# Optimization experiments

Hardware: AMD Instinct MI355X
Metric: run time of the kernel (lower is better)

The kernel has to match this reference:

```python
import jax, jax.numpy as jnp
import numpy as np

B, N, D = 1, 2048, 512        # batch, query seq len, model dim
H, DH = 8, 64                 # heads, head dim
MEM = 512                     # cached XL memory tokens (one window segment)
KV = N + MEM                  # kv sequence length
WINDOW = 512                  # block / sliding-window size
LOOKBACK = 1                  # lookback_blocks
N_EP = 4                      # number of episodes
SCALE = DH ** -0.5


def _rope(t, pos):
    # t: [b,h,l,dh], pos: [l]  (GPT-NeoX half rotation)
    dh = t.shape[-1]
    inv_freq = 1.0 / (10000.0 ** (jnp.arange(0, dh, 2, dtype=jnp.float32) / dh))
    freqs = pos.astype(jnp.float32)[:, None] * inv_freq[None, :]   # [l, dh/2]
    freqs = jnp.concatenate([freqs, freqs], axis=-1)               # [l, dh]
    cos, sin = jnp.cos(freqs), jnp.sin(freqs)
    x1, x2 = jnp.split(t, 2, axis=-1)
    rotated = jnp.concatenate([-x2, x1], axis=-1)
    return t * cos + rotated * sin


def setup_inputs() -> dict:
    key = jax.random.key(0)
    ks = jax.random.split(key, 8)
    x = jax.random.normal(ks[0], (B, N, D), jnp.float32)
    cache_k = jax.random.normal(ks[1], (B, H, MEM, DH), jnp.float32)
    cache_v = jax.random.normal(ks[2], (B, H, MEM, DH), jnp.float32)
    episode_ids = jnp.sort(jax.random.randint(ks[3], (B, KV), 0, N_EP, dtype=jnp.int32), axis=-1)
    Wq = jax.random.normal(ks[4], (D, H * DH), jnp.float32) * 0.02
    Wkv = jax.random.normal(ks[5], (D, 2 * H * DH), jnp.float32) * 0.02
    Wg = jax.random.normal(ks[6], (D, H), jnp.float32) * 0.02
    Wo = jax.random.normal(ks[7], (H * DH, D), jnp.float32) * 0.02
    return dict(x=x, cache_k=cache_k, cache_v=cache_v, episode_ids=episode_ids,
                Wq=Wq, Wkv=Wkv, Wg=Wg, Wo=Wo)


def _xl_mask(episode_ids):
    # mirrors create_xl_mask: causal + block window with lookback + intra-episode
    offset = KV - N
    q_pos = offset + jnp.arange(N)          # [N]
    k_pos = jnp.arange(KV)                  # [KV]
    causal = q_pos[:, None] >= k_pos[None, :]
    bq = q_pos // WINDOW
    bk = k_pos // WINDOW
    block = (bq[:, None] >= bk[None, :]) & (bq[:, None] <= bk[None, :] + LOOKBACK)
    intra_ep = episode_ids[:, q_pos][:, :, None] == episode_ids[:, None, :]  # [B,N,KV]
    return (causal & block)[None] & intra_ep                                 # [B,N,KV]


def reference(x, cache_k, cache_v, episode_ids, Wq, Wkv, Wg, Wo):
    b, n, _ = x.shape
    offset = KV - N

    q = (x @ Wq).reshape(b, n, H, DH).transpose(0, 2, 1, 3)          # [b,h,n,dh]
    kv = (x @ Wkv).reshape(b, n, 2, H, DH)
    k_new = kv[:, :, 0].transpose(0, 2, 1, 3)                        # [b,h,n,dh]
    v_new = kv[:, :, 1].transpose(0, 2, 1, 3)

    k = jnp.concatenate([cache_k, k_new], axis=2)                    # [b,h,kv,dh]
    v = jnp.concatenate([cache_v, v_new], axis=2)

    q = _rope(q, offset + jnp.arange(n))
    k = _rope(k, jnp.arange(KV))

    scores = jnp.einsum('bhnd,bhmd->bhnm', q, k) * SCALE             # [b,h,n,kv]
    mask = _xl_mask(episode_ids)[:, None]                            # [b,1,n,kv]
    scores = jnp.where(mask, scores, jnp.finfo(scores.dtype).min)
    attn = jax.nn.softmax(scores, axis=-1)

    out = jnp.einsum('bhnm,bhmd->bhnd', attn, v)                     # [b,h,n,dh]

    gates = jax.nn.sigmoid(x @ Wg).transpose(0, 2, 1)[..., None]     # [b,h,n,1]
    out = out * gates

    out = out.transpose(0, 2, 1, 3).reshape(b, n, H * DH)            # merge heads
    return out @ Wo                                                  # [b,n,d]
```

## Files before the change

kernel.cpp:

```cpp
#include <hip/hip_runtime.h>
#include <math.h>

#define NQ     2048
#define DMODEL 512
#define NH     8
#define DHD    64
#define MEMT   512
#define KVT    2560
#define QSCALE 0.125f
#define NEGF   (-1e30f)

typedef unsigned short u16;
typedef __bf16 bf16x8 __attribute__((ext_vector_type(8)));
typedef float  f32x4  __attribute__((ext_vector_type(4)));
typedef u16    u16x8  __attribute__((ext_vector_type(8)));
typedef u16    u16x4  __attribute__((ext_vector_type(4)));

__device__ __forceinline__ u16 f2bf(float f) {
    union { float f; unsigned u; } v; v.f = f;
    unsigned r = (v.u + 0x7FFFu + ((v.u >> 16) & 1u)) >> 16;
    return (u16)r;
}

__global__ __launch_bounds__(256) void prep(const float* __restrict__ x,
                                            const float* __restrict__ Wq,
                                            const float* __restrict__ Wkv,
                                            const float* __restrict__ Wo,
                                            const float* __restrict__ Wg,
                                            u16* __restrict__ xb,
                                            u16* __restrict__ Wt,
                                            u16* __restrict__ Wot,
                                            float* __restrict__ gates,
                                            float2* __restrict__ cs) {
    __shared__ float tile[64][65];
    int bx = blockIdx.x, tid = threadIdx.x;

    if (bx >= 384) {
        int t = (bx - 384) * 256 + tid;
        int pos = t >> 5, j = t & 31;
        float invf = exp2f(-(float)j * (13.287712379549449f / 32.f));
        float ss, sc;
        sincosf((float)pos * invf, &ss, &sc);
        cs[t] = make_float2(sc, ss);
        return;
    }
    if (bx >= 320) {
        int t = (bx - 320) * 256 + tid;
        int n = t >> 3, hh = t & 7;
        float acc = 0.f;
        for (int k = 0; k < DMODEL; k += 4) {
            float4 xv = *(const float4*)&x[n * DMODEL + k];
            acc += xv.x * Wg[(k + 0) * NH + hh] + xv.y * Wg[(k + 1) * NH + hh]
                 + xv.z * Wg[(k + 2) * NH + hh] + xv.w * Wg[(k + 3) * NH + hh];
        }
        gates[hh * NQ + n] = 1.f / (1.f + __expf(-acc));
        return;
    }
    if (bx < 64) {
        int base4 = bx * 4096;
#pragma unroll
        for (int u = 0; u < 16; ++u) {
            int i4 = base4 + u * 256 + tid;
            float4 v = ((const float4*)x)[i4];
            u16x4 o = { f2bf(v.x), f2bf(v.y), f2bf(v.z), f2bf(v.w) };
            *(u16x4*)&xb[i4 * 4] = o;
        }
        return;
    }
    int tt = bx - 64;
    bool isQKV = (tt < 192);
    int tc, tr;
    if (isQKV) { tc = tt % 24; tr = tt / 24; }
    else       { tt -= 192; tc = tt & 7; tr = tt >> 3; }

    int rr = tid >> 4, c4 = (tid & 15) * 4;
#pragma unroll
    for (int u = 0; u < 4; ++u) {
        int row = u * 16 + rr;
        int k = tr * 64 + row;
        int c = tc * 64 + c4;
        float4 v;
        if (isQKV) v = (c < 512) ? *(const float4*)&Wq[k * 512 + c]
                                 : *(const float4*)&Wkv[k * 1024 + (c - 512)];
        else       v = *(const float4*)&Wo[k * 512 + c];
        tile[row][c4 + 0] = v.x; tile[row][c4 + 1] = v.y;
        tile[row][c4 + 2] = v.z; tile[row][c4 + 3] = v.w;
    }
    __syncthreads();
#pragma unroll
    for (int u = 0; u < 4; ++u) {
        int trow = u * 16 + rr;
        u16x4 o;
#pragma unroll
        for (int i = 0; i < 4; ++i) o[i] = f2bf(tile[c4 + i][trow]);
        int t_glob = tc * 64 + trow;
        int k_glob = tr * 64 + c4;
        if (isQKV) *(u16x4*)&Wt[t_glob * 512 + k_glob] = o;
        else       *(u16x4*)&Wot[t_glob * 512 + k_glob] = o;
    }
}

__global__ __launch_bounds__(256) void kv_prep(const float* __restrict__ cache_k,
                                               const float* __restrict__ cache_v,
                                               const u16* __restrict__ vn,
                                               const float2* __restrict__ cs,
                                               u16* __restrict__ kb,
                                               u16* __restrict__ vt) {
    __shared__ u16 tile[64][66];
    int h = blockIdx.y, bx = blockIdx.x;
    int tid = threadIdx.x;

    if (bx < 8) {
        int r0 = bx * 64;
#pragma unroll
        for (int u = 0; u < 8; ++u) {
            int idx = u * 256 + tid;
            int row = idx >> 5, j = idx & 31;
            int r = r0 + row;
            float a = cache_k[(h * MEMT + r) * DHD + j];
            float b = cache_k[(h * MEMT + r) * DHD + 32 + j];
            float2 csv = cs[r * 32 + j];
            kb[(h * KVT + r) * DHD + j]      = f2bf(a * csv.x - b * csv.y);
            kb[(h * KVT + r) * DHD + 32 + j] = f2bf(b * csv.x + a * csv.y);
        }
        return;
    }

    int tb = bx - 8;
    int rr = tid >> 4, c4 = (tid & 15) * 4;
    if (tb < 8) {
        int r0 = tb * 64;
#pragma unroll
        for (int u = 0; u < 4; ++u) {
            int row = u * 16 + rr;
            float4 v = *(const float4*)&cache_v[(h * MEMT + r0 + row) * DHD + c4];
            tile[row][c4 + 0] = f2bf(v.x); tile[row][c4 + 1] = f2bf(v.y);
            tile[row][c4 + 2] = f2bf(v.z); tile[row][c4 + 3] = f2bf(v.w);
        }
    } else {
        int n0 = (tb - 8) * 64;
#pragma unroll
        for (int u = 0; u < 4; ++u) {
            int row = u * 16 + rr;
            u16x4 v = *(const u16x4*)&vn[(h * NQ + n0 + row) * DHD + c4];
            tile[row][c4 + 0] = v[0]; tile[row][c4 + 1] = v[1];
            tile[row][c4 + 2] = v[2]; tile[row][c4 + 3] = v[3];
        }
    }
    __syncthreads();
    int kvbase = tb * 64;
#pragma unroll
    for (int u = 0; u < 4; ++u) {
        int d = u * 16 + rr;
        u16x4 o = { tile[c4 + 0][d], tile[c4 + 1][d], tile[c4 + 2][d], tile[c4 + 3][d] };
        *(u16x4*)&vt[(h * DHD + d) * KVT + kvbase + c4] = o;
    }
}

template<int MODE>
__global__ __launch_bounds__(256) void gemm_mfma(const u16* __restrict__ A,
                                                 const u16* __restrict__ Bt,
                                                 const float2* __restrict__ cs,
                                                 u16* __restrict__ o_q,
                                                 u16* __restrict__ o_k,
                                                 u16* __restrict__ o_v,
                                                 float* __restrict__ o_f) {
    int bx = blockIdx.x, by = blockIdx.y;
    int tid = threadIdx.x;
    int w = tid >> 6, lane = tid & 63;
    int lr = lane & 15, lg = lane >> 4;
    int rowbase = by * 64 + (w >> 1) * 32;
    int colbase = bx * 64 + (w & 1) * 16;

    f32x4 acc[2][2];
#pragma unroll
    for (int i = 0; i < 2; ++i)
#pragma unroll
        for (int j = 0; j < 2; ++j) { f32x4 z = {0.f, 0.f, 0.f, 0.f}; acc[i][j] = z; }

    const u16* a0 = A + (rowbase + lr) * 512 + lg * 8;
    const u16* a1 = a0 + 16 * 512;
    const u16* b0 = Bt + (colbase + lr) * 512 + lg * 8;
    const u16* b1 = b0 + 32 * 512;

#pragma unroll 4
    for (int k0 = 0; k0 < 512; k0 += 32) {
        bf16x8 fa0 = __builtin_bit_cast(bf16x8, *(const u16x8*)(a0 + k0));
        bf16x8 fa1 = __builtin_bit_cast(bf16x8, *(const u16x8*)(a1 + k0));
        bf16x8 fb0 = __builtin_bit_cast(bf16x8, *(const u16x8*)(b0 + k0));
        bf16x8 fb1 = __builtin_bit_cast(bf16x8, *(const u16x8*)(b1 + k0));
        acc[0][0] = __builtin_amdgcn_mfma_f32_16x16x32_bf16(fa0, fb0, acc[0][0], 0, 0, 0);
        acc[0][1] = __builtin_amdgcn_mfma_f32_16x16x32_bf16(fa0, fb1, acc[0][1], 0, 0, 0);
        acc[1][0] = __builtin_amdgcn_mfma_f32_16x16x32_bf16(fa1, fb0, acc[1][0], 0, 0, 0);
        acc[1][1] = __builtin_amdgcn_mfma_f32_16x16x32_bf16(fa1, fb1, acc[1][1], 0, 0, 0);
    }

    if (MODE == 1) {
#pragma unroll
        for (int rt = 0; rt < 2; ++rt)
#pragma unroll
            for (int r = 0; r < 4; ++r) {
                int n = rowbase + rt * 16 + lg * 4 + r;
                o_f[n * DMODEL + colbase + lr]      = acc[rt][0][r];
                o_f[n * DMODEL + colbase + 32 + lr] = acc[rt][1][r];
            }
        return;
    }

    int j = (colbase & 63) + lr;
    int region = bx >> 3;
    int h = bx & 7;
#pragma unroll
    for (int rt = 0; rt < 2; ++rt)
#pragma unroll
        for (int r = 0; r < 4; ++r) {
            int n = rowbase + rt * 16 + lg * 4 + r;
            float a = acc[rt][0][r], b = acc[rt][1][r];
            if (region == 2) {
                o_v[(h * NQ + n) * DHD + j]      = f2bf(a);
                o_v[(h * NQ + n) * DHD + 32 + j] = f2bf(b);
            } else {
                float2 csv = cs[(512 + n) * 32 + j];
                u16 e0 = f2bf(a * csv.x - b * csv.y);
                u16 e1 = f2bf(b * csv.x + a * csv.y);
                if (region == 0) {
                    o_q[(h * NQ + n) * DHD + j]      = e0;
                    o_q[(h * NQ + n) * DHD + 32 + j] = e1;
                } else {
                    o_k[(h * KVT + 512 + n) * DHD + j]      = e0;
                    o_k[(h * KVT + 512 + n) * DHD + 32 + j] = e1;
                }
            }
        }
}

#define LOADK(BK, BEP, C0)                                                     \
  _Pragma("unroll")                                                            \
  for (int t = 0; t < 4; ++t) {                                                \
    const u16* kr = kb + ((h * KVT + (C0) + t * 16 + lr) * DHD + lg * 8);      \
    BK[t][0] = __builtin_bit_cast(bf16x8, *(const u16x8*)kr);                  \
    BK[t][1] = __builtin_bit_cast(bf16x8, *(const u16x8*)(kr + 32));           \
    BEP[t] = ep[(C0) + t * 16 + lr];                                           \
  }

#define DO_CHUNK(C0, BK, BEP, PREF, NBK, NBEP)                                 \
  {                                                                            \
    bf16x8 bV[4][2];                                                           \
    _Pragma("unroll")                                                          \
    for (int t = 0; t < 4; ++t) {                                              \
      const u16* vr = vtb + ((h * DHD + t * 16 + lr) * KVT + (C0) + lg * 8);   \
      bV[t][0] = __builtin_bit_cast(bf16x8, *(const u16x8*)vr);                \
      bV[t][1] = __builtin_bit_cast(bf16x8, *(const u16x8*)(vr + 32));         \
    }                                                                          \
    f32x4 s[4];                                                                \
    _Pragma("unroll")                                                          \
    for (int t = 0; t < 4; ++t) {                                              \
      f32x4 z = {0.f, 0.f, 0.f, 0.f};                                          \
      s[t] = __builtin_amdgcn_mfma_f32_16x16x32_bf16(aQ[0], BK[t][0], z, 0, 0, 0); \
      s[t] = __builtin_amdgcn_mfma_f32_16x16x32_bf16(aQ[1], BK[t][1], s[t], 0, 0, 0); \
    }                                                                          \
    if (PREF) { LOADK(NBK, NBEP, (C0) + 64) }                                  \
    float rmax[4] = {NEGF, NEGF, NEGF, NEGF};                                  \
    _Pragma("unroll")                                                          \
    for (int t = 0; t < 4; ++t) {                                              \
      int key = (C0) + t * 16 + lr;                                            \
      int ek = BEP[t];                                                         \
      _Pragma("unroll")                                                        \
      for (int r = 0; r < 4; ++r) {                                            \
        bool vld = (key <= qpos[r]) && (ek == epq[r]);                         \
        float sv = vld ? s[t][r] * QSCALE : NEGF;                              \
        s[t][r] = sv;                                                          \
        rmax[r] = fmaxf(rmax[r], sv);                                          \
      }                                                                        \
    }                                                                          \
    _Pragma("unroll")                                                          \
    for (int mm = 1; mm < 16; mm <<= 1) {                                      \
      _Pragma("unroll")                                                        \
      for (int r = 0; r < 4; ++r)                                              \
        rmax[r] = fmaxf(rmax[r], __shfl_xor(rmax[r], mm, 64));                 \
    }                                                                          \
    float alpha[4];                                                            \
    _Pragma("unroll")                                                          \
    for (int r = 0; r < 4; ++r) {                                              \
      float mn = fmaxf(mrun[r], rmax[r]);                                      \
      alpha[r] = __expf(mrun[r] - mn);                                         \
      mrun[r] = mn;                                                            \
      lsum[r] *= alpha[r];                                                     \
    }                                                                          \
    _Pragma("unroll")                                                          \
    for (int t = 0; t < 4; ++t)                                                \
      _Pragma("unroll")                                                        \
      for (int r = 0; r < 4; ++r) o[t][r] *= alpha[r];                         \
    float psum[4] = {0.f, 0.f, 0.f, 0.f};                                      \
    _Pragma("unroll")                                                          \
    for (int t = 0; t < 4; ++t) {                                              \
      _Pragma("unroll")                                                        \
      for (int r = 0; r < 4; ++r) {                                            \
        float sv = s[t][r];                                                    \
        float p = (sv <= -1e29f) ? 0.f : __expf(sv - mrun[r]);                 \
        psum[r] += p;                                                          \
        int qq = lg * 4 + r;                                                   \
        int kk2 = t * 16 + lr;                                                 \
        pl[qq * 64 + (kk2 ^ ((qq & 7) << 3))] = f2bf(p);                       \
      }                                                                        \
    }                                                                          \
    _Pragma("unroll")                                                          \
    for (int mm = 1; mm < 16; mm <<= 1) {                                      \
      _Pragma("unroll")                                                        \
      for (int r = 0; r < 4; ++r) psum[r] += __shfl_xor(psum[r], mm, 64);      \
    }                                                                          \
    _Pragma("unroll")                                                          \
    for (int r = 0; r < 4; ++r) lsum[r] += psum[r];                            \
    bf16x8 aP[2];                                                              \
    {                                                                          \
      int sw = (lr & 7) << 3;                                                  \
      aP[0] = __builtin_bit_cast(bf16x8, *(const u16x8*)&pl[lr * 64 + ((lg * 8) ^ sw)]);        \
      aP[1] = __builtin_bit_cast(bf16x8, *(const u16x8*)&pl[lr * 64 + ((32 + lg * 8) ^ sw)]);   \
    }                                                                          \
    _Pragma("unroll")                                                          \
    for (int t = 0; t < 4; ++t) {                                              \
      o[t] = __builtin_amdgcn_mfma_f32_16x16x32_bf16(aP[0], bV[t][0], o[t], 0, 0, 0); \
      o[t] = __builtin_amdgcn_mfma_f32_16x16x32_bf16(aP[1], bV[t][1], o[t], 0, 0, 0); \
    }                                                                          \
  }

__global__ __launch_bounds__(256, 2) void attn_mfma(const u16* __restrict__ qb,
                                                    const u16* __restrict__ kb,
                                                    const u16* __restrict__ vtb,
                                                    const float* __restrict__ gates,
                                                    const int* __restrict__ ep,
                                                    u16* __restrict__ outp) {
    __shared__ u16 plds[4][16 * 64];
    __shared__ float o_l[2][16][68];
    __shared__ float ml_l[2][2][16];

    int h = blockIdx.y;
    int q0 = blockIdx.x * 32;
    int tid = threadIdx.x;
    int w = tid >> 6, lane = tid & 63;
    int lr = lane & 15, lg = lane >> 4;
    int qsub = w & 1, kvh = w >> 1;
    int qbase = q0 + qsub * 16;
    u16* pl = plds[w];

    bf16x8 aQ[2];
    {
        const u16* qrow = qb + ((h * NQ + qbase + lr) * DHD + lg * 8);
        aQ[0] = __builtin_bit_cast(bf16x8, *(const u16x8*)qrow);
        aQ[1] = __builtin_bit_cast(bf16x8, *(const u16x8*)(qrow + 32));
    }

    int qpos[4], epq[4];
    float gq[4];
#pragma unroll
    for (int r = 0; r < 4; ++r) {
        int q = qbase + lg * 4 + r;
        qpos[r] = 512 + q;
        epq[r] = ep[512 + q];
        gq[r] = gates[h * NQ + q];
    }

    f32x4 o[4];
    float mrun[4], lsum[4];
#pragma unroll
    for (int t = 0; t < 4; ++t) { f32x4 z = {0.f,0.f,0.f,0.f}; o[t] = z; }
#pragma unroll
    for (int r = 0; r < 4; ++r) { mrun[r] = NEGF; lsum[r] = 0.f; }

    int c_lo = q0 & ~511;
    int nch = (544 + (q0 & 511) + 63) >> 6;
    int n0 = nch >> 1;
    int my_n = kvh ? (nch - n0) : n0;
    int c0 = c_lo + (kvh ? (n0 << 6) : 0);

    bf16x8 bKA[4][2], bKB[4][2];
    int epA[4], epB[4];

    LOADK(bKA, epA, c0)
    int ci = 0;
    while (true) {
        bool more = (ci + 1 < my_n);
        DO_CHUNK(c0, bKA, epA, more, bKB, epB)
        ++ci; c0 += 64;
        if (!more) break;
        bool more2 = (ci + 1 < my_n);
        DO_CHUNK(c0, bKB, epB, more2, bKA, epA)
        ++ci; c0 += 64;
        if (!more2) break;
    }

    if (kvh == 1) {
#pragma unroll
        for (int r = 0; r < 4; ++r) {
            ml_l[qsub][0][lg * 4 + r] = mrun[r];
            ml_l[qsub][1][lg * 4 + r] = lsum[r];
        }
#pragma unroll
        for (int t = 0; t < 4; ++t)
#pragma unroll
            for (int r = 0; r < 4; ++r)
                o_l[qsub][lg * 4 + r][t * 16 + lr] = o[t][r];
    }
    __syncthreads();
    if (kvh == 0) {
#pragma unroll
        for (int r = 0; r < 4; ++r) {
            int row = lg * 4 + r;
            float m1 = ml_l[qsub][0][row], l1 = ml_l[qsub][1][row];
            float m0 = mrun[r], l0 = lsum[r];
            float mm2 = fmaxf(m0, m1);
            float f0 = (m0 <= -1e29f) ? 0.f : __expf(m0 - mm2);
            float f1 = (m1 <= -1e29f) ? 0.f : __expf(m1 - mm2);
            float lt = l0 * f0 + l1 * f1;
            float inv = gq[r] / lt;
            int q = qbase + row;
#pragma unroll
            for (int t = 0; t < 4; ++t) {
                float o1 = o_l[qsub][row][t * 16 + lr];
                outp[q * DMODEL + h * DHD + t * 16 + lr] =
                    f2bf((o[t][r] * f0 + o1 * f1) * inv);
            }
        }
    }
}

extern "C" void kernel_launch(void* const* d_in, const int* in_sizes, int n_in,
                              void* d_out, int out_size, void* d_ws, size_t ws_size,
                              hipStream_t stream) {
    const float* x       = (const float*)d_in[0];
    const float* cache_k = (const float*)d_in[1];
    const float* cache_v = (const float*)d_in[2];
    const int*   ep      = (const int*)  d_in[3];
    const float* Wq      = (const float*)d_in[4];
    const float* Wkv     = (const float*)d_in[5];
    const float* Wg      = (const float*)d_in[6];
    const float* Wo      = (const float*)d_in[7];
    float* out = (float*)d_out;

    u16* u = (u16*)d_ws;
    u16* x_bf    = u;
    u16* Wt      = x_bf + 1048576;
    u16* Wot     = Wt + 786432;
    u16* q_bf    = Wot + 262144;
    u16* k_bf    = q_bf + 1048576;
    u16* vn_bf   = k_bf + 1310720;
    u16* vT      = vn_bf + 1048576;
    u16* attn_bf = vT + 1310720;
    float*  gatesw = (float*)(attn_bf + 1048576);
    float2* cs     = (float2*)(gatesw + 16384);

    prep<<<704, 256, 0, stream>>>(x, Wq, Wkv, Wo, Wg, x_bf, Wt, Wot, gatesw, cs);
    gemm_mfma<0><<<dim3(24, 32), 256, 0, stream>>>(x_bf, Wt, cs, q_bf, k_bf, vn_bf, nullptr);
    kv_prep<<<dim3(48, 8), 256, 0, stream>>>(cache_k, cache_v, vn_bf, cs, k_bf, vT);
    attn_mfma<<<dim3(64, 8), 256, 0, stream>>>(q_bf, k_bf, vT, gatesw, ep, attn_bf);
    gemm_mfma<1><<<dim3(8, 32), 256, 0, stream>>>(attn_bf, Wot, nullptr, nullptr, nullptr, nullptr, out);
}
```

Baseline: 154.8 us.

## Fuse all stages into one persistent kernel with software grid barriers

Replaces the five separate kernel launches (prep, QKV GEMM, kv_prep, attention, output GEMM) with a single persistent kernel of 512 blocks. Phases are separated by a flag-based grid barrier in global memory. The QKV GEMM epilogue now writes V directly in transposed layout, which removes the intermediate vn buffer and its separate transpose pass. The goal is to cut launch overhead and inter-kernel gaps. In exchange it relies on all 512 blocks being co-resident, adds barrier spin cost, and reuses flags tags across calls.

```diff
diff --git a/kernel.cpp b/kernel.cpp
--- a/kernel.cpp
+++ b/kernel.cpp
@@ -9,6 +9,7 @@
 #define KVT    2560
 #define QSCALE 0.125f
 #define NEGF   (-1e30f)
+#define NBLK   512
 
 typedef unsigned short u16;
 typedef __bf16 bf16x8 __attribute__((ext_vector_type(8)));
@@ -22,216 +23,33 @@
     return (u16)r;
 }
 
-__global__ __launch_bounds__(256) void prep(const float* __restrict__ x,
-                                            const float* __restrict__ Wq,
-                                            const float* __restrict__ Wkv,
-                                            const float* __restrict__ Wo,
-                                            const float* __restrict__ Wg,
-                                            u16* __restrict__ xb,
-                                            u16* __restrict__ Wt,
-                                            u16* __restrict__ Wot,
-                                            float* __restrict__ gates,
-                                            float2* __restrict__ cs) {
-    __shared__ float tile[64][65];
-    int bx = blockIdx.x, tid = threadIdx.x;
-
-    if (bx >= 384) {
-        int t = (bx - 384) * 256 + tid;
-        int pos = t >> 5, j = t & 31;
-        float invf = exp2f(-(float)j * (13.287712379549449f / 32.f));
-        float ss, sc;
-        sincosf((float)pos * invf, &ss, &sc);
-        cs[t] = make_float2(sc, ss);
-        return;
-    }
-    if (bx >= 320) {
-        int t = (bx - 320) * 256 + tid;
-        int n = t >> 3, hh = t & 7;
-        float acc = 0.f;
-        for (int k = 0; k < DMODEL; k += 4) {
-            float4 xv = *(const float4*)&x[n * DMODEL + k];
-            acc += xv.x * Wg[(k + 0) * NH + hh] + xv.y * Wg[(k + 1) * NH + hh]
-                 + xv.z * Wg[(k + 2) * NH + hh] + xv.w * Wg[(k + 3) * NH + hh];
-        }
-        gates[hh * NQ + n] = 1.f / (1.f + __expf(-acc));
-        return;
-    }
-    if (bx < 64) {
-        int base4 = bx * 4096;
-#pragma unroll
-        for (int u = 0; u < 16; ++u) {
-            int i4 = base4 + u * 256 + tid;
-            float4 v = ((const float4*)x)[i4];
-            u16x4 o = { f2bf(v.x), f2bf(v.y), f2bf(v.z), f2bf(v.w) };
-            *(u16x4*)&xb[i4 * 4] = o;
-        }
-        return;
-    }
-    int tt = bx - 64;
-    bool isQKV = (tt < 192);
-    int tc, tr;
-    if (isQKV) { tc = tt % 24; tr = tt / 24; }
-    else       { tt -= 192; tc = tt & 7; tr = tt >> 3; }
-
-    int rr = tid >> 4, c4 = (tid & 15) * 4;
-#pragma unroll
-    for (int u = 0; u < 4; ++u) {
-        int row = u * 16 + rr;
-        int k = tr * 64 + row;
-        int c = tc * 64 + c4;
-        float4 v;
-        if (isQKV) v = (c < 512) ? *(const float4*)&Wq[k * 512 + c]
-                                 : *(const float4*)&Wkv[k * 1024 + (c - 512)];
-        else       v = *(const float4*)&Wo[k * 512 + c];
-        tile[row][c4 + 0] = v.x; tile[row][c4 + 1] = v.y;
-        tile[row][c4 + 2] = v.z; tile[row][c4 + 3] = v.w;
+__device__ __forceinline__ void gridbar(int* flags, int tag) {
+    __syncthreads();
+    int bid = blockIdx.x, tid = threadIdx.x;
+    if (tid == 0)
+        __hip_atomic_store(&flags[bid], tag, __ATOMIC_RELEASE, __HIP_MEMORY_SCOPE_AGENT);
+    if (bid == 0) {
+        __shared__ int nd;
+        for (;;) {
+            if (tid == 0) nd = 0;
+            __syncthreads();
+            int bad = 0;
+            for (int j = tid; j < NBLK; j += 256)
+                if (__hip_atomic_load(&flags[j], __ATOMIC_ACQUIRE, __HIP_MEMORY_SCOPE_AGENT) != tag) { bad = 1; break; }
+            if (bad) nd = 1;
+            __syncthreads();
+            if (nd == 0) break;
+            __builtin_amdgcn_s_sleep(2);
+        }
+        if (tid == 0)
+            __hip_atomic_store(&flags[NBLK], tag, __ATOMIC_RELEASE, __HIP_MEMORY_SCOPE_AGENT);
+    } else {
+        if (tid == 0) {
+            while (__hip_atomic_load(&flags[NBLK], __ATOMIC_ACQUIRE, __HIP_MEMORY_SCOPE_AGENT) != tag)
+                __builtin_amdgcn_s_sleep(2);
+        }
     }
     __syncthreads();
-#pragma unroll
-    for (int u = 0; u < 4; ++u) {
-        int trow = u * 16 + rr;
-        u16x4 o;
-#pragma unroll
-        for (int i = 0; i < 4; ++i) o[i] = f2bf(tile[c4 + i][trow]);
-        int t_glob = tc * 64 + trow;
-        int k_glob = tr * 64 + c4;
-        if (isQKV) *(u16x4*)&Wt[t_glob * 512 + k_glob] = o;
-        else       *(u16x4*)&Wot[t_glob * 512 + k_glob] = o;
-    }
-}
-
-__global__ __launch_bounds__(256) void kv_prep(const float* __restrict__ cache_k,
-                                               const float* __restrict__ cache_v,
-                                               const u16* __restrict__ vn,
-                                               const float2* __restrict__ cs,
-                                               u16* __restrict__ kb,
-                                               u16* __restrict__ vt) {
-    __shared__ u16 tile[64][66];
-    int h = blockIdx.y, bx = blockIdx.x;
-    int tid = threadIdx.x;
-
-    if (bx < 8) {
-        int r0 = bx * 64;
-#pragma unroll
-        for (int u = 0; u < 8; ++u) {
-            int idx = u * 256 + tid;
-            int row = idx >> 5, j = idx & 31;
-            int r = r0 + row;
-            float a = cache_k[(h * MEMT + r) * DHD + j];
-            float b = cache_k[(h * MEMT + r) * DHD + 32 + j];
-            float2 csv = cs[r * 32 + j];
-            kb[(h * KVT + r) * DHD + j]      = f2bf(a * csv.x - b * csv.y);
-            kb[(h * KVT + r) * DHD + 32 + j] = f2bf(b * csv.x + a * csv.y);
-        }
-        return;
-    }
-
-    int tb = bx - 8;
-    int rr = tid >> 4, c4 = (tid & 15) * 4;
-    if (tb < 8) {
-        int r0 = tb * 64;
-#pragma unroll
-        for (int u = 0; u < 4; ++u) {
-            int row = u * 16 + rr;
-            float4 v = *(const float4*)&cache_v[(h * MEMT + r0 + row) * DHD + c4];
-            tile[row][c4 + 0] = f2bf(v.x); tile[row][c4 + 1] = f2bf(v.y);
-            tile[row][c4 + 2] = f2bf(v.z); tile[row][c4 + 3] = f2bf(v.w);
-        }
-    } else {
-        int n0 = (tb - 8) * 64;
-#pragma unroll
-        for (int u = 0; u < 4; ++u) {
-            int row = u * 16 + rr;
-            u16x4 v = *(const u16x4*)&vn[(h * NQ + n0 + row) * DHD + c4];
-            tile[row][c4 + 0] = v[0]; tile[row][c4 + 1] = v[1];
-            tile[row][c4 + 2] = v[2]; tile[row][c4 + 3] = v[3];
-        }
-    }
-    __syncthreads();
-    int kvbase = tb * 64;
-#pragma unroll
-    for (int u = 0; u < 4; ++u) {
-        int d = u * 16 + rr;
-        u16x4 o = { tile[c4 + 0][d], tile[c4 + 1][d], tile[c4 + 2][d], tile[c4 + 3][d] };
-        *(u16x4*)&vt[(h * DHD + d) * KVT + kvbase + c4] = o;
-    }
-}
-
-template<int MODE>
-__global__ __launch_bounds__(256) void gemm_mfma(const u16* __restrict__ A,
-                                                 const u16* __restrict__ Bt,
-                                                 const float2* __restrict__ cs,
-                                                 u16* __restrict__ o_q,
-                                                 u16* __restrict__ o_k,
-                                                 u16* __restrict__ o_v,
-                                                 float* __restrict__ o_f) {
-    int bx = blockIdx.x, by = blockIdx.y;
-    int tid = threadIdx.x;
-    int w = tid >> 6, lane = tid & 63;
-    int lr = lane & 15, lg = lane >> 4;
-    int rowbase = by * 64 + (w >> 1) * 32;
-    int colbase = bx * 64 + (w & 1) * 16;
-
-    f32x4 acc[2][2];
-#pragma unroll
-    for (int i = 0; i < 2; ++i)
-#pragma unroll
-        for (int j = 0; j < 2; ++j) { f32x4 z = {0.f, 0.f, 0.f, 0.f}; acc[i][j] = z; }
-
-    const u16* a0 = A + (rowbase + lr) * 512 + lg * 8;
-    const u16* a1 = a0 + 16 * 512;
-    const u16* b0 = Bt + (colbase + lr) * 512 + lg * 8;
-    const u16* b1 = b0 + 32 * 512;
-
-#pragma unroll 4
-    for (int k0 = 0; k0 < 512; k0 += 32) {
-        bf16x8 fa0 = __builtin_bit_cast(bf16x8, *(const u16x8*)(a0 + k0));
-        bf16x8 fa1 = __builtin_bit_cast(bf16x8, *(const u16x8*)(a1 + k0));
-        bf16x8 fb0 = __builtin_bit_cast(bf16x8, *(const u16x8*)(b0 + k0));
-        bf16x8 fb1 = __builtin_bit_cast(bf16x8, *(const u16x8*)(b1 + k0));
-        acc[0][0] = __builtin_amdgcn_mfma_f32_16x16x32_bf16(fa0, fb0, acc[0][0], 0, 0, 0);
-        acc[0][1] = __builtin_amdgcn_mfma_f32_16x16x32_bf16(fa0, fb1, acc[0][1], 0, 0, 0);
-        acc[1][0] = __builtin_amdgcn_mfma_f32_16x16x32_bf16(fa1, fb0, acc[1][0], 0, 0, 0);
-        acc[1][1] = __builtin_amdgcn_mfma_f32_16x16x32_bf16(fa1, fb1, acc[1][1], 0, 0, 0);
-    }
-
-    if (MODE == 1) {
-#pragma unroll
-        for (int rt = 0; rt < 2; ++rt)
-#pragma unroll
-            for (int r = 0; r < 4; ++r) {
-                int n = rowbase + rt * 16 + lg * 4 + r;
-                o_f[n * DMODEL + colbase + lr]      = acc[rt][0][r];
-                o_f[n * DMODEL + colbase + 32 + lr] = acc[rt][1][r];
-            }
-        return;
-    }
-
-    int j = (colbase & 63) + lr;
-    int region = bx >> 3;
-    int h = bx & 7;
-#pragma unroll
-    for (int rt = 0; rt < 2; ++rt)
-#pragma unroll
-        for (int r = 0; r < 4; ++r) {
-            int n = rowbase + rt * 16 + lg * 4 + r;
-            float a = acc[rt][0][r], b = acc[rt][1][r];
-            if (region == 2) {
-                o_v[(h * NQ + n) * DHD + j]      = f2bf(a);
-                o_v[(h * NQ + n) * DHD + 32 + j] = f2bf(b);
-            } else {
-                float2 csv = cs[(512 + n) * 32 + j];
-                u16 e0 = f2bf(a * csv.x - b * csv.y);
-                u16 e1 = f2bf(b * csv.x + a * csv.y);
-                if (region == 0) {
-                    o_q[(h * NQ + n) * DHD + j]      = e0;
-                    o_q[(h * NQ + n) * DHD + 32 + j] = e1;
-                } else {
-                    o_k[(h * KVT + 512 + n) * DHD + j]      = e0;
-                    o_k[(h * KVT + 512 + n) * DHD + 32 + j] = e1;
-                }
-            }
-        }
 }
 
 #define LOADK(BK, BEP, C0)                                                     \
@@ -324,102 +142,307 @@
     }                                                                          \
   }
 
-__global__ __launch_bounds__(256, 2) void attn_mfma(const u16* __restrict__ qb,
-                                                    const u16* __restrict__ kb,
-                                                    const u16* __restrict__ vtb,
-                                                    const float* __restrict__ gates,
-                                                    const int* __restrict__ ep,
-                                                    u16* __restrict__ outp) {
-    __shared__ u16 plds[4][16 * 64];
-    __shared__ float o_l[2][16][68];
-    __shared__ float ml_l[2][2][16];
-
-    int h = blockIdx.y;
-    int q0 = blockIdx.x * 32;
-    int tid = threadIdx.x;
-    int w = tid >> 6, lane = tid & 63;
-    int lr = lane & 15, lg = lane >> 4;
-    int qsub = w & 1, kvh = w >> 1;
-    int qbase = q0 + qsub * 16;
-    u16* pl = plds[w];
-
-    bf16x8 aQ[2];
+__global__ __launch_bounds__(256, 2) void mega(
+    const float* __restrict__ x, const float* __restrict__ cache_k,
+    const float* __restrict__ cache_v, const int* __restrict__ ep,
+    const float* __restrict__ Wq, const float* __restrict__ Wkv,
+    const float* __restrict__ Wg, const float* __restrict__ Wo,
+    u16* __restrict__ xb, u16* __restrict__ Wt, u16* __restrict__ Wot,
+    u16* __restrict__ qb, u16* __restrict__ kb, u16* __restrict__ vtb,
+    u16* __restrict__ attnb, float* __restrict__ gates,
+    float2* __restrict__ cs, int* __restrict__ flags,
+    float* __restrict__ outf)
+{
+    __shared__ char smem[17408];
+    const int bid = blockIdx.x, tid = threadIdx.x;
+    const int w = tid >> 6, lane = tid & 63;
+    const int lr = lane & 15, lg = lane >> 4;
+
+    for (int unit = bid; unit < 576; unit += NBLK) {
+        if (unit < 64) {
+            int base4 = unit * 4096;
+#pragma unroll
+            for (int u = 0; u < 16; ++u) {
+                int i4 = base4 + u * 256 + tid;
+                float4 v = ((const float4*)x)[i4];
+                u16x4 o4 = { f2bf(v.x), f2bf(v.y), f2bf(v.z), f2bf(v.w) };
+                *(u16x4*)&xb[i4 * 4] = o4;
+            }
+        } else if (unit < 320) {
+            __syncthreads();
+            float (*tile)[65] = (float(*)[65])smem;
+            int tt = unit - 64;
+            bool isQKV = (tt < 192);
+            int tc, tr;
+            if (isQKV) { tc = tt % 24; tr = tt / 24; }
+            else       { tt -= 192; tc = tt & 7; tr = tt >> 3; }
+            int rr = tid >> 4, c4 = (tid & 15) * 4;
+#pragma unroll
+            for (int u = 0; u < 4; ++u) {
+                int row = u * 16 + rr;
+                int k = tr * 64 + row, c = tc * 64 + c4;
+                float4 v;
+                if (isQKV) v = (c < 512) ? *(const float4*)&Wq[k * 512 + c]
+                                         : *(const float4*)&Wkv[k * 1024 + (c - 512)];
+                else       v = *(const float4*)&Wo[k * 512 + c];
+                tile[row][c4 + 0] = v.x; tile[row][c4 + 1] = v.y;
+                tile[row][c4 + 2] = v.z; tile[row][c4 + 3] = v.w;
+            }
+            __syncthreads();
+#pragma unroll
+            for (int u = 0; u < 4; ++u) {
+                int trow = u * 16 + rr;
+                u16x4 o4;
+#pragma unroll
+                for (int i = 0; i < 4; ++i) o4[i] = f2bf(tile[c4 + i][trow]);
+                int tg = tc * 64 + trow, kg = tr * 64 + c4;
+                if (isQKV) *(u16x4*)&Wt[tg * 512 + kg] = o4;
+                else       *(u16x4*)&Wot[tg * 512 + kg] = o4;
+            }
+        } else if (unit < 384) {
+            int t = (unit - 320) * 256 + tid;
+            int n = t >> 3, hh = t & 7;
+            float acc = 0.f;
+            for (int k = 0; k < DMODEL; k += 4) {
+                float4 xv = *(const float4*)&x[n * DMODEL + k];
+                acc += xv.x * Wg[(k + 0) * NH + hh] + xv.y * Wg[(k + 1) * NH + hh]
+                     + xv.z * Wg[(k + 2) * NH + hh] + xv.w * Wg[(k + 3) * NH + hh];
+            }
+            gates[hh * NQ + n] = 1.f / (1.f + __expf(-acc));
+        } else if (unit < 512) {
+            int tu = unit - 384;
+#pragma unroll
+            for (int kk = 0; kk < 3; ++kk) {
+                int e = kk * 256 + tid;
+                if (e < 640) {
+                    int idx = tu * 640 + e;
+                    int pos = idx >> 5, j = idx & 31;
+                    float invf = exp2f(-(float)j * (13.287712379549449f / 32.f));
+                    float ss, sc;
+                    sincosf((float)pos * invf, &ss, &sc);
+                    cs[idx] = make_float2(sc, ss);
+                }
+            }
+        } else {
+            __syncthreads();
+            u16 (*tile)[66] = (u16(*)[66])smem;
+            int uu = unit - 512;
+            int tb = uu & 7, h = uu >> 3;
+            int rr = tid >> 4, c4 = (tid & 15) * 4;
+            int r0 = tb * 64;
+#pragma unroll
+            for (int u = 0; u < 4; ++u) {
+                int row = u * 16 + rr;
+                float4 v = *(const float4*)&cache_v[(h * MEMT + r0 + row) * DHD + c4];
+                tile[row][c4 + 0] = f2bf(v.x); tile[row][c4 + 1] = f2bf(v.y);
+                tile[row][c4 + 2] = f2bf(v.z); tile[row][c4 + 3] = f2bf(v.w);
+            }
+            __syncthreads();
+#pragma unroll
+            for (int u = 0; u < 4; ++u) {
+                int d = u * 16 + rr;
+                u16x4 o4 = { tile[c4 + 0][d], tile[c4 + 1][d], tile[c4 + 2][d], tile[c4 + 3][d] };
+                *(u16x4*)&vtb[(h * DHD + d) * KVT + r0 + c4] = o4;
+            }
+        }
+    }
+    gridbar(flags, 0x7A5A0001);
+
+    for (int u2 = bid; u2 < 832; u2 += NBLK) {
+        if (u2 < 768) {
+            int bx = u2 % 24, by = u2 / 24;
+            int rowbase = by * 64 + (w >> 1) * 32;
+            int colbase = bx * 64 + (w & 1) * 16;
+            f32x4 acc[2][2];
+#pragma unroll
+            for (int i = 0; i < 2; ++i)
+#pragma unroll
+                for (int j = 0; j < 2; ++j) { f32x4 z = {0.f,0.f,0.f,0.f}; acc[i][j] = z; }
+            const u16* a0 = xb + (rowbase + lr) * 512 + lg * 8;
+            const u16* a1 = a0 + 16 * 512;
+            const u16* b0 = Wt + (colbase + lr) * 512 + lg * 8;
+            const u16* b1 = b0 + 32 * 512;
+#pragma unroll 4
+            for (int k0 = 0; k0 < 512; k0 += 32) {
+                bf16x8 fa0 = __builtin_bit_cast(bf16x8, *(const u16x8*)(a0 + k0));
+                bf16x8 fa1 = __builtin_bit_cast(bf16x8, *(const u16x8*)(a1 + k0));
+                bf16x8 fb0 = __builtin_bit_cast(bf16x8, *(const u16x8*)(b0 + k0));
+                bf16x8 fb1 = __builtin_bit_cast(bf16x8, *(const u16x8*)(b1 + k0));
+                acc[0][0] = __builtin_amdgcn_mfma_f32_16x16x32_bf16(fa0, fb0, acc[0][0], 0, 0, 0);
+                acc[0][1] = __builtin_amdgcn_mfma_f32_16x16x32_bf16(fa0, fb1, acc[0][1], 0, 0, 0);
+                acc[1][0] = __builtin_amdgcn_mfma_f32_16x16x32_bf16(fa1, fb0, acc[1][0], 0, 0, 0);
+                acc[1][1] = __builtin_amdgcn_mfma_f32_16x16x32_bf16(fa1, fb1, acc[1][1], 0, 0, 0);
+            }
+            int j = (colbase & 63) + lr;
+            int region = bx >> 3;
+            int h = bx & 7;
+            if (region == 2) {
+                __syncthreads();
+                u16 (*vtile)[72] = (u16(*)[72])smem;
+#pragma unroll
+                for (int rt = 0; rt < 2; ++rt)
+#pragma unroll
+                    for (int r = 0; r < 4; ++r) {
+                        int rl = (w >> 1) * 32 + rt * 16 + lg * 4 + r;
+                        vtile[rl][j]      = f2bf(acc[rt][0][r]);
+                        vtile[rl][j + 32] = f2bf(acc[rt][1][r]);
+                    }
+                __syncthreads();
+                int rr = tid >> 4, c4 = (tid & 15) * 4;
+#pragma unroll
+                for (int u = 0; u < 4; ++u) {
+                    int d = u * 16 + rr;
+                    u16x4 o4 = { vtile[c4 + 0][d], vtile[c4 + 1][d], vtile[c4 + 2][d], vtile[c4 + 3][d] };
+                    *(u16x4*)&vtb[(h * DHD + d) * KVT + 512 + by * 64 + c4] = o4;
+                }
+            } else {
+#pragma unroll
+                for (int rt = 0; rt < 2; ++rt)
+#pragma unroll
+                    for (int r = 0; r < 4; ++r) {
+                        int n = rowbase + rt * 16 + lg * 4 + r;
+                        float a = acc[rt][0][r], b = acc[rt][1][r];
+                        float2 csv = cs[(512 + n) * 32 + j];
+                        u16 e0 = f2bf(a * csv.x - b * csv.y);
+                        u16 e1 = f2bf(b * csv.x + a * csv.y);
+                        if (region == 0) {
+                            qb[(h * NQ + n) * DHD + j]      = e0;
+                            qb[(h * NQ + n) * DHD + 32 + j] = e1;
+                        } else {
+                            kb[(h * KVT + 512 + n) * DHD + j]      = e0;
+                            kb[(h * KVT + 512 + n) * DHD + 32 + j] = e1;
+                        }
+                    }
+            }
+        } else {
+            int uu = u2 - 768;
+            int r0 = (uu & 7) * 64, h = uu >> 3;
+#pragma unroll
+            for (int u = 0; u < 8; ++u) {
+                int idx = u * 256 + tid;
+                int row = idx >> 5, j = idx & 31;
+                int r = r0 + row;
+                float a = cache_k[(h * MEMT + r) * DHD + j];
+                float b = cache_k[(h * MEMT + r) * DHD + 32 + j];
+                float2 csv = cs[r * 32 + j];
+                kb[(h * KVT + r) * DHD + j]      = f2bf(a * csv.x - b * csv.y);
+                kb[(h * KVT + r) * DHD + 32 + j] = f2bf(b * csv.x + a * csv.y);
+            }
+        }
+    }
+    gridbar(flags, 0x7A5A0002);
+
     {
-        const u16* qrow = qb + ((h * NQ + qbase + lr) * DHD + lg * 8);
-        aQ[0] = __builtin_bit_cast(bf16x8, *(const u16x8*)qrow);
-        aQ[1] = __builtin_bit_cast(bf16x8, *(const u16x8*)(qrow + 32));
+        u16* plds = (u16*)smem;
+        float* o_lf = (float*)(smem + 8192);
+        float* ml_lf = (float*)(smem + 16896);
+        int h = bid >> 6;
+        int q0 = (bid & 63) * 32;
+        int qsub = w & 1, kvh = w >> 1;
+        int qbase = q0 + qsub * 16;
+        u16* pl = plds + w * 1024;
+
+        bf16x8 aQ[2];
+        {
+            const u16* qrow = qb + ((h * NQ + qbase + lr) * DHD + lg * 8);
+            aQ[0] = __builtin_bit_cast(bf16x8, *(const u16x8*)qrow);
+            aQ[1] = __builtin_bit_cast(bf16x8, *(const u16x8*)(qrow + 32));
+        }
+        int qpos[4], epq[4];
+        float gq[4];
+#pragma unroll
+        for (int r = 0; r < 4; ++r) {
+            int q = qbase + lg * 4 + r;
+            qpos[r] = 512 + q;
+            epq[r] = ep[512 + q];
+            gq[r] = gates[h * NQ + q];
+        }
+        f32x4 o[4];
+        float mrun[4], lsum[4];
+#pragma unroll
+        for (int t = 0; t < 4; ++t) { f32x4 z = {0.f,0.f,0.f,0.f}; o[t] = z; }
+#pragma unroll
+        for (int r = 0; r < 4; ++r) { mrun[r] = NEGF; lsum[r] = 0.f; }
+
+        int c_lo = q0 & ~511;
+        int nch = (544 + (q0 & 511) + 63) >> 6;
+        int n0 = nch >> 1;
+        int my_n = kvh ? (nch - n0) : n0;
+        int c0 = c_lo + (kvh ? (n0 << 6) : 0);
+
+        bf16x8 bKA[4][2], bKB[4][2];
+        int epA[4], epB[4];
+        LOADK(bKA, epA, c0)
+        int ci = 0;
+        while (true) {
+            bool more = (ci + 1 < my_n);
+            DO_CHUNK(c0, bKA, epA, more, bKB, epB)
+            ++ci; c0 += 64;
+            if (!more) break;
+            bool more2 = (ci + 1 < my_n);
+            DO_CHUNK(c0, bKB, epB, more2, bKA, epA)
+            ++ci; c0 += 64;
+            if (!more2) break;
+        }
+
+        if (kvh == 1) {
+#pragma unroll
+            for (int r = 0; r < 4; ++r) {
+                ml_lf[(qsub * 2 + 0) * 16 + lg * 4 + r] = mrun[r];
+                ml_lf[(qsub * 2 + 1) * 16 + lg * 4 + r] = lsum[r];
+            }
+#pragma unroll
+            for (int t = 0; t < 4; ++t)
+#pragma unroll
+                for (int r = 0; r < 4; ++r)
+                    o_lf[(qsub * 16 + lg * 4 + r) * 68 + t * 16 + lr] = o[t][r];
+        }
+        __syncthreads();
+        if (kvh == 0) {
+#pragma unroll
+            for (int r = 0; r < 4; ++r) {
+                int row = lg * 4 + r;
+                float m1 = ml_lf[(qsub * 2 + 0) * 16 + row];
+                float l1 = ml_lf[(qsub * 2 + 1) * 16 + row];
+                float m0 = mrun[r], l0 = lsum[r];
+                float mm2 = fmaxf(m0, m1);
+                float f0 = (m0 <= -1e29f) ? 0.f : __expf(m0 - mm2);
+                float f1 = (m1 <= -1e29f) ? 0.f : __expf(m1 - mm2);
+                float lt = l0 * f0 + l1 * f1;
+                float inv = gq[r] / lt;
+                int q = qbase + row;
+#pragma unroll
+                for (int t = 0; t < 4; ++t) {
+                    float o1 = o_lf[(qsub * 16 + row) * 68 + t * 16 + lr];
+                    attnb[q * DMODEL + h * DHD + t * 16 + lr] =
+                        f2bf((o[t][r] * f0 + o1 * f1) * inv);
+                }
+            }
+        }
     }
-
-    int qpos[4], epq[4];
-    float gq[4];
-#pragma unroll
-    for (int r = 0; r < 4; ++r) {
-        int q = qbase + lg * 4 + r;
-        qpos[r] = 512 + q;
-        epq[r] = ep[512 + q];
-        gq[r] = gates[h * NQ + q];
-    }
-
-    f32x4 o[4];
-    float mrun[4], lsum[4];
-#pragma unroll
-    for (int t = 0; t < 4; ++t) { f32x4 z = {0.f,0.f,0.f,0.f}; o[t] = z; }
-#pragma unroll
-    for (int r = 0; r < 4; ++r) { mrun[r] = NEGF; lsum[r] = 0.f; }
-
-    int c_lo = q0 & ~511;
-    int nch = (544 + (q0 & 511) + 63) >> 6;
-    int n0 = nch >> 1;
-    int my_n = kvh ? (nch - n0) : n0;
-    int c0 = c_lo + (kvh ? (n0 << 6) : 0);
-
-    bf16x8 bKA[4][2], bKB[4][2];
-    int epA[4], epB[4];
-
-    LOADK(bKA, epA, c0)
-    int ci = 0;
-    while (true) {
-        bool more = (ci + 1 < my_n);
-        DO_CHUNK(c0, bKA, epA, more, bKB, epB)
-        ++ci; c0 += 64;
-        if (!more) break;
-        bool more2 = (ci + 1 < my_n);
-        DO_CHUNK(c0, bKB, epB, more2, bKA, epA)
-        ++ci; c0 += 64;
-        if (!more2) break;
-    }
-
-    if (kvh == 1) {
+    gridbar(flags, 0x7A5A0003);
+
+    if (bid < 512) {
+        int bx = bid & 7, by = bid >> 3;
+        int rowbase = by * 32 + (w >> 1) * 16;
+        int colbase = bx * 64 + (w & 1) * 16;
+        f32x4 acc0 = {0.f,0.f,0.f,0.f}, acc1 = {0.f,0.f,0.f,0.f};
+        const u16* a0 = attnb + (rowbase + lr) * 512 + lg * 8;
+        const u16* b0 = Wot + (colbase + lr) * 512 + lg * 8;
+        const u16* b1 = b0 + 32 * 512;
+#pragma unroll 4
+        for (int k0 = 0; k0 < 512; k0 += 32) {
+            bf16x8 fa  = __builtin_bit_cast(bf16x8, *(const u16x8*)(a0 + k0));
+            bf16x8 fb0 = __builtin_bit_cast(bf16x8, *(const u16x8*)(b0 + k0));
+            bf16x8 fb1 = __builtin_bit_cast(bf16x8, *(const u16x8*)(b1 + k0));
+            acc0 = __builtin_amdgcn_mfma_f32_16x16x32_bf16(fa, fb0, acc0, 0, 0, 0);
+            acc1 = __builtin_amdgcn_mfma_f32_16x16x32_bf16(fa, fb1, acc1, 0, 0, 0);
+        }
 #pragma unroll
         for (int r = 0; r < 4; ++r) {
-            ml_l[qsub][0][lg * 4 + r] = mrun[r];
-            ml_l[qsub][1][lg * 4 + r] = lsum[r];
-        }
-#pragma unroll
-        for (int t = 0; t < 4; ++t)
-#pragma unroll
-            for (int r = 0; r < 4; ++r)
-                o_l[qsub][lg * 4 + r][t * 16 + lr] = o[t][r];
-    }
-    __syncthreads();
-    if (kvh == 0) {
-#pragma unroll
-        for (int r = 0; r < 4; ++r) {
-            int row = lg * 4 + r;
-            float m1 = ml_l[qsub][0][row], l1 = ml_l[qsub][1][row];
-            float m0 = mrun[r], l0 = lsum[r];
-            float mm2 = fmaxf(m0, m1);
-            float f0 = (m0 <= -1e29f) ? 0.f : __expf(m0 - mm2);
-            float f1 = (m1 <= -1e29f) ? 0.f : __expf(m1 - mm2);
-            float lt = l0 * f0 + l1 * f1;
-            float inv = gq[r] / lt;
-            int q = qbase + row;
-#pragma unroll
-            for (int t = 0; t < 4; ++t) {
-                float o1 = o_l[qsub][row][t * 16 + lr];
-                outp[q * DMODEL + h * DHD + t * 16 + lr] =
-                    f2bf((o[t][r] * f0 + o1 * f1) * inv);
-            }
+            int n = rowbase + lg * 4 + r;
+            outf[n * DMODEL + colbase + lr]      = acc0[r];
+            outf[n * DMODEL + colbase + 32 + lr] = acc1[r];
         }
     }
 }
@@ -443,15 +466,13 @@
     u16* Wot     = Wt + 786432;
     u16* q_bf    = Wot + 262144;
     u16* k_bf    = q_bf + 1048576;
-    u16* vn_bf   = k_bf + 1310720;
-    u16* vT      = vn_bf + 1048576;
+    u16* vT      = k_bf + 1310720;
     u16* attn_bf = vT + 1310720;
     float*  gatesw = (float*)(attn_bf + 1048576);
     float2* cs     = (float2*)(gatesw + 16384);
-
-    prep<<<704, 256, 0, stream>>>(x, Wq, Wkv, Wo, Wg, x_bf, Wt, Wot, gatesw, cs);
-    gemm_mfma<0><<<dim3(24, 32), 256, 0, stream>>>(x_bf, Wt, cs, q_bf, k_bf, vn_bf, nullptr);
-    kv_prep<<<dim3(48, 8), 256, 0, stream>>>(cache_k, cache_v, vn_bf, cs, k_bf, vT);
-    attn_mfma<<<dim3(64, 8), 256, 0, stream>>>(q_bf, k_bf, vT, gatesw, ep, attn_bf);
-    gemm_mfma<1><<<dim3(8, 32), 256, 0, stream>>>(attn_bf, Wot, nullptr, nullptr, nullptr, nullptr, out);
+    int*    flags  = (int*)(cs + 81920);
+
+    mega<<<NBLK, 256, 0, stream>>>(x, cache_k, cache_v, ep, Wq, Wkv, Wg, Wo,
+                                   x_bf, Wt, Wot, q_bf, k_bf, vT, attn_bf,
+                                   gatesw, cs, flags, out);
 }
```

Measured after the change: 395.8 us. 156% more time.
